# Optimization experiments

Measured on AMD Instinct MI355X. Metric: run time of the kernel, lower is better.

Reference implementation:

```python
import jax, jax.numpy as jnp
import numpy as np

B, S, D, H, F, L, V, SPAN = 4, 1024, 1024, 16, 4096, 4, 32000, 512
DH = D // H
NEG = -1e9


def _ln(x, g, b, eps=1e-12):
    m = x.mean(-1, keepdims=True)
    v = ((x - m) ** 2).mean(-1, keepdims=True)
    return (x - m) * jax.lax.rsqrt(v + eps) * g + b


def setup_inputs() -> dict:
    key = jax.random.key(0)
    ks = iter(jax.random.split(key, 40))
    g = lambda shape: jax.random.normal(next(ks), shape, jnp.float32) * 0.02
    inp = {
        "input_ids": jax.random.randint(next(ks), (B, S), 0, V),
        "segment_ids": jnp.zeros((B, S), jnp.int32),
        "attention_mask": jnp.ones((B, S), jnp.float32),
        "tok_emb": g((V, D)),
        "seg_emb": g((2, D)),
        "emb_ln_g": jnp.ones((D,), jnp.float32),
        "emb_ln_b": jnp.zeros((D,), jnp.float32),
        "rel_emb": g((2 * SPAN, D)),
        "Wq": g((L, D, D)), "bq": jnp.zeros((L, D), jnp.float32),
        "Wk": g((L, D, D)), "bk": jnp.zeros((L, D), jnp.float32),
        "Wv": g((L, D, D)), "bv": jnp.zeros((L, D), jnp.float32),
        "Wo": g((L, D, D)), "bo": jnp.zeros((L, D), jnp.float32),
        "ln1_g": jnp.ones((L, D), jnp.float32), "ln1_b": jnp.zeros((L, D), jnp.float32),
        "W1": g((L, D, F)), "b1": jnp.zeros((L, F), jnp.float32),
        "W2": g((L, F, D)), "b2": jnp.zeros((L, D), jnp.float32),
        "ln2_g": jnp.ones((L, D), jnp.float32), "ln2_b": jnp.zeros((L, D), jnp.float32),
    }
    return inp


def _forward(input_ids, segment_ids, attention_mask, tok_emb, seg_emb, emb_ln_g,
             emb_ln_b, rel_emb, Wq, bq, Wk, bk, Wv, bv, Wo, bo, ln1_g, ln1_b,
             W1, b1, W2, b2, ln2_g, ln2_b):
    # BertEmbedding (max_len=0 => no absolute positions): token + segment, LN, mask
    h = _ln(tok_emb[input_ids] + seg_emb[segment_ids], emb_ln_g, emb_ln_b)
    h = h * attention_mask[..., None]

    # relative positions (bucket_size=0 path): rel[q,k] = q - k, clamped into table
    pos = jnp.arange(S)
    rel = pos[:, None] - pos[None, :]                      # [S,S]
    c2p_idx = jnp.clip(rel + SPAN, 0, 2 * SPAN - 1)        # [S,S]
    p2c_idx = jnp.clip(-rel + SPAN, 0, 2 * SPAN - 1)       # [S,S]
    bias = (1.0 - attention_mask)[:, None, None, :] * NEG  # [B,1,1,S] additive mask

    scale = 1.0 / jnp.sqrt(jnp.asarray(DH * 3, h.dtype))   # scale_factor = 1 + |{c2p,p2c}|

    def layer(h, p):
        wq, bq_, wk, bk_, wv, bv_, wo, bo_, g1, b1n, w1, b1f, w2, b2f, g2, b2n = p
        q = (h @ wq + bq_).reshape(B, S, H, DH)
        k = (h @ wk + bk_).reshape(B, S, H, DH)
        v = (h @ wv + bv_).reshape(B, S, H, DH)
        att = jnp.einsum('bqhd,bkhd->bhqk', q, k) * scale
        # disentangled relative-position bias (shared q/k projections on rel table)
        pos_k = (rel_emb @ wk + bk_).reshape(2 * SPAN, H, DH)
        pos_q = (rel_emb @ wq + bq_).reshape(2 * SPAN, H, DH)
        c2p = jnp.einsum('bqhd,phd->bhqp', q, pos_k) * scale   # [B,H,S,2*SPAN]
        att = att + jnp.take_along_axis(c2p, c2p_idx[None, None], axis=-1)
        p2c = jnp.einsum('bkhd,phd->bhkp', k, pos_q) * scale   # [B,H,S,2*SPAN]
        att = att + jnp.swapaxes(
            jnp.take_along_axis(p2c, p2c_idx[None, None], axis=-1), -1, -2)
        probs = jax.nn.softmax(att + bias, axis=-1)
        ctx = jnp.einsum('bhqk,bkhd->bqhd', probs, v).reshape(B, S, D)
        h = _ln(h + ctx @ wo + bo_, g1, b1n)
        ff = jax.nn.gelu(h @ w1 + b1f, approximate=False) @ w2 + b2f
        return _ln(h + ff, g2, b2n), None

    h, _ = jax.lax.scan(layer, h, (Wq, bq, Wk, bk, Wv, bv, Wo, bo,
                                   ln1_g, ln1_b, W1, b1, W2, b2, ln2_g, ln2_b))
    return h


def reference(input_ids, segment_ids, attention_mask, tok_emb, seg_emb, emb_ln_g,
              emb_ln_b, rel_emb, Wq, bq, Wk, bk, Wv, bv, Wo, bo, ln1_g, ln1_b,
              W1, b1, W2, b2, ln2_g, ln2_b):
    return _forward(input_ids, segment_ids, attention_mask, tok_emb, seg_emb,
                    emb_ln_g, emb_ln_b, rel_emb, Wq, bq, Wk, bk, Wv, bv, Wo, bo,
                    ln1_g, ln1_b, W1, b1, W2, b2, ln2_g, ln2_b)
```

## Files before the change

### kernel.cpp

```cpp
#include <hip/hip_runtime.h>

#define DEV __device__ __forceinline__

typedef __bf16 bf16;
typedef __bf16 bf16x4 __attribute__((ext_vector_type(4)));
typedef __bf16 bf16x8 __attribute__((ext_vector_type(8)));
typedef float f32x4 __attribute__((ext_vector_type(4)));

constexpr int B_ = 4, S_ = 1024, D_ = 1024, H_ = 16, F_ = 4096, L_ = 4, SPAN_ = 512, DH_ = 64;
constexpr float SCALE_ = 0.07216878364870322f;
constexpr float LOG2E_ = 1.4426950408889634f;
constexpr float SCL2_ = SCALE_ * LOG2E_;
constexpr float THR2_ = 11.5f;
constexpr long POSL_ = 32L * 1024 * 64;

DEV void gload_lds16(const void* g, void* l) {
  __builtin_amdgcn_global_load_lds((const __attribute__((address_space(1))) void*)g,
                                   (__attribute__((address_space(3))) void*)l, 16, 0, 0);
}

template <int CTRL>
DEV float dppf(float x) {
  return __builtin_bit_cast(
      float, __builtin_amdgcn_mov_dpp(__builtin_bit_cast(int, x), CTRL, 0xf, 0xf, true));
}
DEV float rowMax16(float v) {
  v = fmaxf(v, dppf<0x128>(v));
  v = fmaxf(v, dppf<0x124>(v));
  v = fmaxf(v, dppf<0x122>(v));
  v = fmaxf(v, dppf<0x121>(v));
  return v;
}
DEV float rowSum16(float v) {
  v += dppf<0x128>(v);
  v += dppf<0x124>(v);
  v += dppf<0x122>(v);
  v += dppf<0x121>(v);
  return v;
}

DEV float blockSum4(float v, volatile float* red) {
#pragma unroll
  for (int o = 32; o; o >>= 1) v += __shfl_xor(v, o);
  if ((threadIdx.x & 63) == 0) red[threadIdx.x >> 6] = v;
  __syncthreads();
  return red[0] + red[1] + red[2] + red[3];
}

DEV bf16x8 lds_frag(const bf16* buf, int row, int chunk) {
  return *(const bf16x8*)((const char*)buf + row * 128 + ((chunk ^ (row & 7)) << 4));
}
DEV bf16x8 rdfrag(const char* base, int row, int chunk) {
  return *(const bf16x8*)(base + row * 128 + ((chunk ^ (row & 7)) << 4));
}

template <int EPI>
__global__ __launch_bounds__(512, 1) void gemm256(
    const bf16* __restrict__ A, const bf16* __restrict__ Bm,
    const float* __restrict__ bias, void* __restrict__ Cout,
    int K, int lda, int ldb, int ldc, long sA, long sB, long sC) {
  extern __shared__ __align__(16) char smem[];

  const int z = blockIdx.z;
  A += (long)z * sA;
  Bm += (long)z * sB;
  const long coff = (long)z * sC;

  const int nwg = gridDim.x * gridDim.y;
  const int flat = blockIdx.y * gridDim.x + blockIdx.x;
  const int qq = nwg >> 3;
  const int swz = (flat & 7) * qq + (flat >> 3);
  const int bx = swz % gridDim.x, by = swz / gridDim.x;
  const int m0 = by * 256, n0 = bx * 256;

  const int tid = threadIdx.x, lane = tid & 63, wave = tid >> 6;
  const int wr = wave >> 2, wc = wave & 3;
  const int fr = lane & 15, fq = lane >> 4;

  f32x4 acc[8][4];
#pragma unroll
  for (int m = 0; m < 8; m++)
#pragma unroll
    for (int n = 0; n < 4; n++) acc[m][n] = f32x4{0.f, 0.f, 0.f, 0.f};

  const int r8 = tid >> 3;
  const int swzel = ((tid & 7) ^ (r8 & 7)) << 3;
  const bf16* ga = A + (long)(m0 + r8) * lda + swzel;
  const bf16* gb = Bm + (long)(n0 + r8) * ldb + swzel;

  const int NT = K >> 6;

  auto stage = [&](int t) {
    const long ko = (long)t * 64;
    char* da = smem + ((t & 1) << 15) + wave * 1024;
    gload_lds16(ga + ko, da);
    gload_lds16(ga + 64 * (long)lda + ko, da + 8192);
    gload_lds16(ga + 128 * (long)lda + ko, da + 16384);
    gload_lds16(ga + 192 * (long)lda + ko, da + 24576);
    char* db = smem + 65536 + ((t & 1) << 15) + wave * 1024;
    gload_lds16(gb + ko, db);
    gload_lds16(gb + 64 * (long)ldb + ko, db + 8192);
    gload_lds16(gb + 128 * (long)ldb + ko, db + 16384);
    gload_lds16(gb + 192 * (long)ldb + ko, db + 24576);
  };

  stage(0);
  asm volatile("s_waitcnt vmcnt(0)" ::: "memory");
  __builtin_amdgcn_s_barrier();

  for (int j = 0; j < NT; j++) {
    const char* Ac = smem + ((j & 1) << 15);
    const char* Bc = smem + 65536 + ((j & 1) << 15);

    if (j + 1 < NT) stage(j + 1);

    bf16x8 af[4][2], bfg[4][2];
#pragma unroll
    for (int m = 0; m < 4; m++) {
      const int ar = wr * 128 + m * 16 + fr;
      af[m][0] = rdfrag(Ac, ar, fq);
      af[m][1] = rdfrag(Ac, ar, 4 + fq);
    }
#pragma unroll
    for (int n = 0; n < 4; n++) {
      const int br = wc * 64 + n * 16 + fr;
      bfg[n][0] = rdfrag(Bc, br, fq);
      bfg[n][1] = rdfrag(Bc, br, 4 + fq);
    }

    __builtin_amdgcn_s_setprio(1);
#pragma unroll
    for (int m = 0; m < 4; m++)
#pragma unroll
      for (int n = 0; n < 4; n++)
#pragma unroll
        for (int kc = 0; kc < 2; kc++)
          acc[m][n] = __builtin_amdgcn_mfma_f32_16x16x32_bf16(af[m][kc], bfg[n][kc],
                                                              acc[m][n], 0, 0, 0);
    __builtin_amdgcn_s_setprio(0);
    __builtin_amdgcn_sched_barrier(0);

#pragma unroll
    for (int m = 0; m < 4; m++) {
      const int ar = wr * 128 + (m + 4) * 16 + fr;
      af[m][0] = rdfrag(Ac, ar, fq);
      af[m][1] = rdfrag(Ac, ar, 4 + fq);
    }
    __builtin_amdgcn_s_setprio(1);
#pragma unroll
    for (int m = 0; m < 4; m++)
#pragma unroll
      for (int n = 0; n < 4; n++)
#pragma unroll
        for (int kc = 0; kc < 2; kc++)
          acc[m + 4][n] = __builtin_amdgcn_mfma_f32_16x16x32_bf16(af[m][kc], bfg[n][kc],
                                                                  acc[m + 4][n], 0, 0, 0);
    __builtin_amdgcn_s_setprio(0);

    asm volatile("s_waitcnt vmcnt(0)" ::: "memory");
    __builtin_amdgcn_s_barrier();
  }

#pragma unroll
  for (int m = 0; m < 8; m++) {
#pragma unroll
    for (int n = 0; n < 4; n++) {
      const int col = n0 + wc * 64 + n * 16 + fr;
      float bval = 0.f;
      if constexpr (EPI == 3 || EPI == 4) bval = bias ? bias[col] : 0.f;
#pragma unroll
      for (int rr = 0; rr < 4; rr++) {
        const int row = m0 + wr * 128 + m * 16 + fq * 4 + rr;
        const long idx = coff + (long)row * ldc + col;
        const float v = acc[m][n][rr];
        if constexpr (EPI == 0) ((float*)Cout)[idx] = v;
        else if constexpr (EPI == 3) ((bf16*)Cout)[idx] = (bf16)(v + bval);
        else if constexpr (EPI == 4) {
          float x = v + bval;
          x = 0.5f * x * (1.f + erff(x * 0.70710678118654752f));
          ((bf16*)Cout)[idx] = (bf16)x;
        }
      }
    }
  }
}

template <int EPI>
__global__ __launch_bounds__(256) void gemm_bt(
    const bf16* __restrict__ A, const bf16* __restrict__ Bm,
    const float* __restrict__ bias, void* __restrict__ Cout,
    int M, int N, int K, int lda, int ldb, int ldc, float alpha,
    long sA, long sB, long sC, long sBias) {
  __shared__ alignas(16) bf16 As[128 * 64];
  __shared__ alignas(16) bf16 Bs[128 * 64];

  const int z = blockIdx.z;
  A += (long)z * sA;
  Bm += (long)z * sB;
  bias += (long)z * sBias;
  const long coff = (long)z * sC;

  const int nwg = gridDim.x * gridDim.y;
  const int flat = blockIdx.y * gridDim.x + blockIdx.x;
  const int qq = nwg >> 3;
  const int swz = (flat & 7) * qq + (flat >> 3);
  const int bx = swz % gridDim.x, by = swz / gridDim.x;

  const int m0 = by * 128, n0 = bx * 128;
  const int tid = threadIdx.x, lane = tid & 63, wave = tid >> 6;
  const int wr = wave >> 1, wc = wave & 1;
  const int fr = lane & 15, fq = lane >> 4;

  f32x4 acc[4][4];
#pragma unroll
  for (int m = 0; m < 4; m++)
#pragma unroll
    for (int n = 0; n < 4; n++) acc[m][n] = f32x4{0.f, 0.f, 0.f, 0.f};

  const int r8 = tid >> 3;
  const int swzel = ((tid & 7) ^ (r8 & 7)) << 3;
  const bf16* ga = A + (long)(m0 + r8) * lda + swzel;
  const bf16* gb = Bm + (long)(n0 + r8) * ldb + swzel;
  const int swzrd = fr & 7;

  for (int k0 = 0; k0 < K; k0 += 64) {
#pragma unroll
    for (int i = 0; i < 4; i++)
      gload_lds16(ga + (long)i * 32 * lda + k0, (char*)As + i * 4096 + wave * 1024);
#pragma unroll
    for (int i = 0; i < 4; i++)
      gload_lds16(gb + (long)i * 32 * ldb + k0, (char*)Bs + i * 4096 + wave * 1024);
    __syncthreads();
#pragma unroll
    for (int kc = 0; kc < 2; kc++) {
      bf16x8 af[4], bfv[4];
#pragma unroll
      for (int m = 0; m < 4; m++)
        af[m] = *(const bf16x8*)((char*)As + (wr * 64 + m * 16 + fr) * 128 +
                                 (((kc * 4 + fq) ^ swzrd) << 4));
#pragma unroll
      for (int n = 0; n < 4; n++)
        bfv[n] = *(const bf16x8*)((char*)Bs + (wc * 64 + n * 16 + fr) * 128 +
                                  (((kc * 4 + fq) ^ swzrd) << 4));
#pragma unroll
      for (int m = 0; m < 4; m++)
#pragma unroll
        for (int n = 0; n < 4; n++)
          acc[m][n] = __builtin_amdgcn_mfma_f32_16x16x32_bf16(af[m], bfv[n], acc[m][n], 0, 0, 0);
    }
    __syncthreads();
  }

#pragma unroll
  for (int m = 0; m < 4; m++) {
#pragma unroll
    for (int n = 0; n < 4; n++) {
      const int col = n0 + wc * 64 + n * 16 + fr;
      float bval = 0.f;
      if constexpr (EPI == 3 || EPI == 4 || EPI == 5) bval = bias ? bias[col] : 0.f;
#pragma unroll
      for (int rr = 0; rr < 4; rr++) {
        const int row = m0 + wr * 64 + m * 16 + fq * 4 + rr;
        const long idx = coff + (long)row * ldc + col;
        const float v = acc[m][n][rr];
        if constexpr (EPI == 0) ((float*)Cout)[idx] = v * alpha;
        else if constexpr (EPI == 3) ((bf16*)Cout)[idx] = (bf16)(v + bval);
        else if constexpr (EPI == 4) {
          float x = v + bval;
          x = 0.5f * x * (1.f + erff(x * 0.70710678118654752f));
          ((bf16*)Cout)[idx] = (bf16)x;
        } else if constexpr (EPI == 5) {
          const long pidx = coff + ((long)(col >> 6) * 1024 + row) * 64 + (col & 63);
          ((bf16*)Cout)[pidx] = (bf16)(v + bval);
        }
      }
    }
  }
}

__global__ __launch_bounds__(256) void repack_kv(const bf16* __restrict__ qkv,
                                                 bf16* __restrict__ kp,
                                                 bf16* __restrict__ vp) {
  const int kt = blockIdx.x, bh = blockIdx.y;
  const int b = bh >> 4, h = bh & 15;
  const int k0 = kt * 64;
  __shared__ bf16 t[64][72];
  const int ty = threadIdx.x >> 3, tx = threadIdx.x & 7;
#pragma unroll
  for (int p = 0; p < 2; p++) {
    const int s = k0 + p * 32 + ty;
    const long base = (long)(b * 1024 + s) * 3072 + h * 64;
    bf16x8 kv = *(const bf16x8*)(qkv + base + 1024 + tx * 8);
    *(bf16x8*)(kp + ((long)(bh * 1024 + s) << 6) + tx * 8) = kv;
    bf16x8 vv = *(const bf16x8*)(qkv + base + 2048 + tx * 8);
    *(bf16x8*)(&t[p * 32 + ty][tx * 8]) = vv;
  }
  __syncthreads();
  const int dh = threadIdx.x >> 2, sc = (threadIdx.x & 3) * 16;
  bf16 tmp[16];
#pragma unroll
  for (int j = 0; j < 16; j++) tmp[j] = t[sc + j][dh];
  bf16* dst = vp + ((long)(bh * 16 + kt) << 12) + dh * 64 + sc;
  *(bf16x8*)dst = *(bf16x8*)tmp;
  *(bf16x8*)(dst + 8) = *(bf16x8*)(tmp + 8);
}

__global__ __launch_bounds__(256) void attn_fused(
    const bf16* __restrict__ qkv, const bf16* __restrict__ kp,
    const bf16* __restrict__ vp, const bf16* __restrict__ pospk,
    const float* __restrict__ mask, bf16* __restrict__ ctx) {
  const int id = blockIdx.x;
  const int xcd = id & 7, sub = id >> 3;
  const int bh = xcd + 8 * (sub >> 4);
  const int qt = sub & 15;
  const int b = bh >> 4, h = bh & 15;
  const int q0 = qt * 64;
  const int tid = threadIdx.x, wave = tid >> 6, lane = tid & 63;
  const int fr = lane & 15, fq = lane >> 4;

  __shared__ alignas(16) char smem[79360];
  bf16* PXk = (bf16*)smem;
  char* p_l = smem;
  bf16* PXq = (bf16*)(smem + 16384);
  bf16* Ks = (bf16*)(smem + 32768);
  bf16* Vs = (bf16*)(smem + 40960);
  bf16* c2p_T = (bf16*)(smem + 49152);
  bf16* p2c_T = (bf16*)(smem + 61952);

  const bf16* posq = pospk + ((long)h << 16);
  const bf16* posk = pospk + ((long)(16 + h) << 16);
  const bf16* kbase = kp + ((long)bh << 16);
  const bf16* vbase = vp + ((long)bh << 16);

  bf16x8 qa[2];
  {
    const bf16* qrow = qkv + (long)(b * 1024 + q0 + wave * 16 + fr) * 3072 + h * 64;
    qa[0] = *(const bf16x8*)(qrow + fq * 8);
    qa[1] = *(const bf16x8*)(qrow + 32 + fq * 8);
  }

  f32x4 o[4];
#pragma unroll
  for (int n = 0; n < 4; n++) o[n] = f32x4{0.f, 0.f, 0.f, 0.f};
  float m_r[4], l_r[4];
#pragma unroll
  for (int r = 0; r < 4; r++) { m_r[r] = -1e30f; l_r[r] = 0.f; }

  char* pl_base = p_l + wave * 2048;
  bf16* c2p_w = c2p_T + wave * 1600;
  const int wbyte = wave * 1024;

  for (int kt = 0; kt < 16; kt++) {
    const int k0 = kt * 64;

    __syncthreads();
    {
      const int j0k = q0 - k0 + 449;
      const int j0q = k0 - q0 + 449;
#pragma unroll
      for (int c = 0; c < 4; c++) {
        const int u = c * 256 + tid;
        const int rr = u >> 3;
        const int sel = (((u & 7) ^ (rr & 7)) << 3);
        int jk = j0k + rr;
        jk = jk < 0 ? 0 : (jk > 1023 ? 1023 : jk);
        gload_lds16(posk + ((long)jk << 6) + sel, (char*)PXk + c * 4096 + wbyte);
        int jq = j0q + rr;
        jq = jq < 0 ? 0 : (jq > 1023 ? 1023 : jq);
        gload_lds16(posq + ((long)jq << 6) + sel, (char*)PXq + c * 4096 + wbyte);
      }
#pragma unroll
      for (int c = 0; c < 2; c++) {
        const int u = c * 256 + tid;
        const int rr = u >> 3;
        const int sel = (((u & 7) ^ (rr & 7)) << 3);
        gload_lds16(kbase + ((long)(k0 + rr) << 6) + sel, (char*)Ks + c * 4096 + wbyte);
        gload_lds16(vbase + ((long)kt << 12) + ((long)rr << 6) + sel,
                    (char*)Vs + c * 4096 + wbyte);
      }
    }
    __syncthreads();

    bf16x8 ka[2];
    ka[0] = lds_frag(Ks, wave * 16 + fr, fq);
    ka[1] = lds_frag(Ks, wave * 16 + fr, 4 + fq);
    __builtin_amdgcn_s_setprio(1);
    {
      f32x4 cw[5];
#pragma unroll
      for (int t = 0; t < 5; t++) cw[t] = f32x4{0.f, 0.f, 0.f, 0.f};
#pragma unroll
      for (int kc = 0; kc < 2; kc++)
#pragma unroll
        for (int t = 0; t < 5; t++) {
          const bf16x8 pb = lds_frag(PXk, wave * 16 + t * 16 + fr, kc * 4 + fq);
          cw[t] = __builtin_amdgcn_mfma_f32_16x16x32_bf16(qa[kc], pb, cw[t], 0, 0, 0);
        }
#pragma unroll
      for (int t = 0; t < 5; t++) {
        bf16x4 pk;
#pragma unroll
        for (int r = 0; r < 4; r++) pk[r] = (bf16)cw[t][r];
        *(bf16x4*)&c2p_w[(t * 16 + fr) * 20 + fq * 4] = pk;
      }
    }
    f32x4 s[4];
#pragma unroll
    for (int n = 0; n < 4; n++) s[n] = f32x4{0.f, 0.f, 0.f, 0.f};
#pragma unroll
    for (int kc = 0; kc < 2; kc++)
#pragma unroll
      for (int n = 0; n < 4; n++) {
        const bf16x8 kb = lds_frag(Ks, n * 16 + fr, kc * 4 + fq);
        s[n] = __builtin_amdgcn_mfma_f32_16x16x32_bf16(qa[kc], kb, s[n], 0, 0, 0);
      }
    {
      f32x4 pw[5];
#pragma unroll
      for (int t = 0; t < 5; t++) pw[t] = f32x4{0.f, 0.f, 0.f, 0.f};
#pragma unroll
      for (int kc = 0; kc < 2; kc++)
#pragma unroll
        for (int t = 0; t < 5; t++) {
          const bf16x8 pb = lds_frag(PXq, (wave + t) * 16 + fr, kc * 4 + fq);
          pw[t] = __builtin_amdgcn_mfma_f32_16x16x32_bf16(ka[kc], pb, pw[t], 0, 0, 0);
        }
#pragma unroll
      for (int t = 0; t < 5; t++) {
        bf16x4 pk;
#pragma unroll
        for (int r = 0; r < 4; r++) pk[r] = (bf16)pw[t][r];
        *(bf16x4*)&p2c_T[((wave + t) * 16 + fr) * 68 + wave * 16 + fq * 4] = pk;
      }
    }
    __builtin_amdgcn_s_setprio(0);
    __syncthreads();

    bf16x8 vb[2][4];
#pragma unroll
    for (int kc = 0; kc < 2; kc++)
#pragma unroll
      for (int n = 0; n < 4; n++) vb[kc][n] = lds_frag(Vs, n * 16 + fr, kc * 4 + fq);

    float st[4][4];
#pragma unroll
    for (int n = 0; n < 4; n++) {
      const int ki = n * 16 + fr;
      const float mb = (1.0f - mask[b * S_ + k0 + ki]) * (-1e9f * LOG2E_);
#pragma unroll
      for (int r = 0; r < 4; r++) {
        const int qi_s = fq * 4 + r;
        const float cv = (float)c2p_w[(qi_s - ki + 63) * 20 + qi_s];
        const float pv = (float)p2c_T[(ki - (wave * 16 + qi_s) + 63) * 68 + ki];
        st[n][r] = (s[n][r] + cv + pv) * SCL2_ + mb;
      }
    }

    float pmax[4];
#pragma unroll
    for (int r = 0; r < 4; r++) {
      float v = fmaxf(fmaxf(st[0][r], st[1][r]), fmaxf(st[2][r], st[3][r]));
      pmax[r] = rowMax16(v);
    }
    const bool ok = (pmax[0] - m_r[0] <= THR2_) && (pmax[1] - m_r[1] <= THR2_) &&
                    (pmax[2] - m_r[2] <= THR2_) && (pmax[3] - m_r[3] <= THR2_);
    if (!__all(ok)) {
#pragma unroll
      for (int r = 0; r < 4; r++) {
        const float mn = fmaxf(m_r[r], pmax[r]);
        const float sc = exp2f(m_r[r] - mn);
        m_r[r] = mn;
        l_r[r] *= sc;
#pragma unroll
        for (int n = 0; n < 4; n++) o[n][r] *= sc;
      }
    }
    float rs[4] = {0.f, 0.f, 0.f, 0.f};
#pragma unroll
    for (int n = 0; n < 4; n++) {
      const int ki = n * 16 + fr;
#pragma unroll
      for (int r = 0; r < 4; r++) {
        const int qi_s = fq * 4 + r;
        const float p = exp2f(st[n][r] - m_r[r]);
        rs[r] += p;
        *(bf16*)(pl_base + qi_s * 128 + ((ki * 2) ^ ((qi_s & 7) << 4))) = (bf16)p;
      }
    }
#pragma unroll
    for (int r = 0; r < 4; r++) l_r[r] += rowSum16(rs[r]);

#pragma unroll
    for (int kc = 0; kc < 2; kc++) {
      const bf16x8 pa =
          *(const bf16x8*)(pl_base + fr * 128 + ((kc * 64 + fq * 16) ^ ((fr & 7) << 4)));
#pragma unroll
      for (int n = 0; n < 4; n++)
        o[n] = __builtin_amdgcn_mfma_f32_16x16x32_bf16(pa, vb[kc][n], o[n], 0, 0, 0);
    }
  }

#pragma unroll
  for (int r = 0; r < 4; r++) {
    const float inv = 1.f / l_r[r];
    const long row = (long)(b * S_ + q0 + wave * 16 + fq * 4 + r) * D_ + h * 64;
#pragma unroll
    for (int n = 0; n < 4; n++) ctx[row + n * 16 + fr] = (bf16)(o[n][r] * inv);
  }
}

__global__ __launch_bounds__(256) void wtrans(const float* __restrict__ W,
                                              bf16* __restrict__ WT, int K, int N,
                                              long sW, long sT) {
  W += (long)blockIdx.z * sW;
  WT += (long)blockIdx.z * sT;
  __shared__ float t[32][33];
  const int n0 = blockIdx.x * 32, k0 = blockIdx.y * 32;
  const int tx = threadIdx.x & 31, ty = threadIdx.x >> 5;
#pragma unroll
  for (int i = ty; i < 32; i += 8) t[i][tx] = W[(long)(k0 + i) * N + n0 + tx];
  __syncthreads();
#pragma unroll
  for (int i = ty; i < 32; i += 8) WT[(long)(n0 + i) * K + k0 + tx] = (bf16)t[tx][i];
}

__global__ __launch_bounds__(256) void f2b(const float* __restrict__ in,
                                           bf16* __restrict__ out, long n) {
  long i = (long)blockIdx.x * 256 + threadIdx.x;
  if (i < n) out[i] = (bf16)in[i];
}

__global__ __launch_bounds__(256) void bias_concat(const float* __restrict__ bq,
                                                   const float* __restrict__ bk,
                                                   const float* __restrict__ bv,
                                                   float* __restrict__ bqkv) {
  const int i = blockIdx.x * 256 + threadIdx.x;
  const int l = i / (3 * D_), s = (i % (3 * D_)) / D_, d = i % D_;
  const float* src = s == 0 ? bq : (s == 1 ? bk : bv);
  bqkv[i] = src[l * D_ + d];
}

__global__ __launch_bounds__(256) void embed_ln(
    const int* __restrict__ ids, const int* __restrict__ segs,
    const float* __restrict__ mask, const float* __restrict__ tok,
    const float* __restrict__ seg, const float* __restrict__ g,
    const float* __restrict__ bta, float* __restrict__ h, bf16* __restrict__ hb) {
  __shared__ float r1[4], r2[4];
  const int t = blockIdx.x;
  const int d4 = threadIdx.x;
  const long tb4 = (long)ids[t] * 256;
  const long sb4 = (long)segs[t] * 256;
  const long b4 = (long)t * 256;
  f32x4 x = ((const f32x4*)tok)[tb4 + d4];
  const f32x4 sv = ((const f32x4*)seg)[sb4 + d4];
#pragma unroll
  for (int r = 0; r < 4; r++) x[r] += sv[r];
  float sm = x[0] + x[1] + x[2] + x[3];
  sm = blockSum4(sm, r1);
  const float mean = sm * (1.f / D_);
  float vs = 0.f;
#pragma unroll
  for (int r = 0; r < 4; r++) {
    const float c = x[r] - mean;
    vs += c * c;
  }
  vs = blockSum4(vs, r2);
  const float rstd = rsqrtf(vs * (1.f / D_) + 1e-12f);
  const float mk = mask[t];
  const f32x4 gv = ((const f32x4*)g)[d4];
  const f32x4 bv = ((const f32x4*)bta)[d4];
  f32x4 y;
  bf16x4 yb;
#pragma unroll
  for (int r = 0; r < 4; r++) {
    y[r] = ((x[r] - mean) * rstd * gv[r] + bv[r]) * mk;
    yb[r] = (bf16)y[r];
  }
  ((f32x4*)h)[b4 + d4] = y;
  *(bf16x4*)&hb[(b4 + d4) * 4] = yb;
}

template <int P>
__global__ __launch_bounds__(256) void ln_residual_red(
    const float* __restrict__ hin, float* __restrict__ hout,
    const float* __restrict__ part, long pstride4,
    const float* __restrict__ bias, const float* __restrict__ g,
    const float* __restrict__ bta, bf16* __restrict__ hb) {
  __shared__ float r1[4], r2[4];
  const int d4 = threadIdx.x;
  const long b4 = (long)blockIdx.x * 256;
  f32x4 x = ((const f32x4*)hin)[b4 + d4];
  const f32x4 bi = ((const f32x4*)bias)[d4];
#pragma unroll
  for (int r = 0; r < 4; r++) x[r] += bi[r];
#pragma unroll
  for (int z = 0; z < P; z++) {
    const f32x4 pv = ((const f32x4*)part)[(long)z * pstride4 + b4 + d4];
#pragma unroll
    for (int r = 0; r < 4; r++) x[r] += pv[r];
  }
  float sm = x[0] + x[1] + x[2] + x[3];
  sm = blockSum4(sm, r1);
  const float mean = sm * (1.f / D_);
  float vs = 0.f;
#pragma unroll
  for (int r = 0; r < 4; r++) {
    const float c = x[r] - mean;
    vs += c * c;
  }
  vs = blockSum4(vs, r2);
  const float rstd = rsqrtf(vs * (1.f / D_) + 1e-12f);
  const f32x4 gv = ((const f32x4*)g)[d4];
  const f32x4 bv = ((const f32x4*)bta)[d4];
  f32x4 y;
  bf16x4 yb;
#pragma unroll
  for (int r = 0; r < 4; r++) {
    y[r] = (x[r] - mean) * rstd * gv[r] + bv[r];
    yb[r] = (bf16)y[r];
  }
  ((f32x4*)hout)[b4 + d4] = y;
  *(bf16x4*)&hb[(b4 + d4) * 4] = yb;
}

extern "C" void kernel_launch(void* const* d_in, const int* in_sizes, int n_in,
                              void* d_out, int out_size, void* d_ws, size_t ws_size,
                              hipStream_t stream) {
  (void)in_sizes; (void)n_in; (void)out_size; (void)ws_size;
  const int* input_ids = (const int*)d_in[0];
  const int* segment_ids = (const int*)d_in[1];
  const float* attention_mask = (const float*)d_in[2];
  const float* tok_emb = (const float*)d_in[3];
  const float* seg_emb = (const float*)d_in[4];
  const float* emb_ln_g = (const float*)d_in[5];
  const float* emb_ln_b = (const float*)d_in[6];
  const float* rel_emb = (const float*)d_in[7];
  const float* Wq = (const float*)d_in[8];
  const float* bq = (const float*)d_in[9];
  const float* Wk = (const float*)d_in[10];
  const float* bk = (const float*)d_in[11];
  const float* Wv = (const float*)d_in[12];
  const float* bv = (const float*)d_in[13];
  const float* Wo = (const float*)d_in[14];
  const float* bo = (const float*)d_in[15];
  const float* ln1_g = (const float*)d_in[16];
  const float* ln1_b = (const float*)d_in[17];
  const float* W1 = (const float*)d_in[18];
  const float* b1 = (const float*)d_in[19];
  const float* W2 = (const float*)d_in[20];
  const float* b2 = (const float*)d_in[21];
  const float* ln2_g = (const float*)d_in[22];
  const float* ln2_b = (const float*)d_in[23];

  const long DD = (long)D_ * D_;
  const long DF = (long)D_ * F_;
  const int D3 = 3 * D_;

  char* ws = (char*)d_ws;
  auto alloc = [&](size_t bytes) {
    char* p = ws;
    ws += (bytes + 255) & ~(size_t)255;
    return p;
  };
  bf16* wqkvT = (bf16*)alloc((size_t)L_ * 3 * DD * 2);
  bf16* woT = (bf16*)alloc((size_t)L_ * DD * 2);
  bf16* w1T = (bf16*)alloc((size_t)L_ * DF * 2);
  bf16* w2T = (bf16*)alloc((size_t)L_ * DF * 2);
  float* bqkv = (float*)alloc((size_t)L_ * 3 * D_ * 4);
  bf16* relb = (bf16*)alloc((size_t)2 * SPAN_ * D_ * 2);
  float* hbuf = (float*)alloc((size_t)B_ * S_ * D_ * 4);
  bf16* hb = (bf16*)alloc((size_t)B_ * S_ * D_ * 2);
  bf16* qkv = (bf16*)alloc((size_t)B_ * S_ * 3 * D_ * 2);
  bf16* kp = (bf16*)alloc((size_t)B_ * H_ * S_ * DH_ * 2);
  bf16* vp = (bf16*)alloc((size_t)B_ * H_ * S_ * DH_ * 2);
  bf16* pospk = (bf16*)alloc((size_t)L_ * POSL_ * 2);
  bf16* ctxb = (bf16*)alloc((size_t)B_ * S_ * D_ * 2);
  bf16* ff1b = (bf16*)alloc((size_t)B_ * S_ * F_ * 2);
  float* kpart = (float*)alloc((size_t)4 * B_ * S_ * D_ * 4);
  const long PSTR = (long)B_ * S_ * D_;

  wtrans<<<dim3(D_ / 32, D_ / 32, L_), 256, 0, stream>>>(Wq, wqkvT + 0 * DD, D_, D_, DD, 3 * DD);
  wtrans<<<dim3(D_ / 32, D_ / 32, L_), 256, 0, stream>>>(Wk, wqkvT + 1 * DD, D_, D_, DD, 3 * DD);
  wtrans<<<dim3(D_ / 32, D_ / 32, L_), 256, 0, stream>>>(Wv, wqkvT + 2 * DD, D_, D_, DD, 3 * DD);
  wtrans<<<dim3(D_ / 32, D_ / 32, L_), 256, 0, stream>>>(Wo, woT, D_, D_, DD, DD);
  wtrans<<<dim3(F_ / 32, D_ / 32, L_), 256, 0, stream>>>(W1, w1T, D_, F_, DF, DF);
  wtrans<<<dim3(D_ / 32, F_ / 32, L_), 256, 0, stream>>>(W2, w2T, F_, D_, DF, DF);
  bias_concat<<<dim3(L_ * 3 * D_ / 256), 256, 0, stream>>>(bq, bk, bv, bqkv);
  f2b<<<dim3((2 * SPAN_ * D_) / 256), 256, 0, stream>>>(rel_emb, relb, (long)2 * SPAN_ * D_);
  gemm_bt<5><<<dim3((2 * D_) / 128, (2 * SPAN_) / 128, L_), 256, 0, stream>>>(
      relb, wqkvT, bqkv, pospk, 2 * SPAN_, 2 * D_, D_, D_, D_, 0, 1.f,
      0, 3 * DD, POSL_, 3 * D_);
  embed_ln<<<dim3(B_ * S_), 256, 0, stream>>>(input_ids, segment_ids, attention_mask,
                                              tok_emb, seg_emb, emb_ln_g, emb_ln_b, hbuf, hb);

  const size_t SH = 131072;

  for (int l = 0; l < L_; ++l) {
    const bf16* wqkv_ = wqkvT + (long)l * 3 * DD;
    const bf16* wo_ = woT + (long)l * DD;
    const bf16* w1_ = w1T + (long)l * DF;
    const bf16* w2_ = w2T + (long)l * DF;
    const float* bqkv_ = bqkv + (long)l * 3 * D_;
    const float* bo_ = bo + (long)l * D_;
    const float* b1_ = b1 + (long)l * F_;
    const float* b2_ = b2 + (long)l * D_;

    gemm_bt<3><<<dim3(D3 / 128, (B_ * S_) / 128, 1), 256, 0, stream>>>(
        hb, wqkv_, bqkv_, qkv, B_ * S_, D3, D_, D_, D_, D3, 1.f, 0, 0, 0, 0);
    repack_kv<<<dim3(16, B_ * H_), 256, 0, stream>>>(qkv, kp, vp);

    attn_fused<<<dim3(1024), 256, 0, stream>>>(qkv, kp, vp, pospk + (long)l * POSL_,
                                               attention_mask, ctxb);

    gemm_bt<0><<<dim3(D_ / 128, (B_ * S_) / 128, 2), 256, 0, stream>>>(
        ctxb, wo_, nullptr, kpart, B_ * S_, D_, D_ / 2, D_, D_, D_, 1.f,
        D_ / 2, D_ / 2, PSTR, 0);
    ln_residual_red<2><<<dim3(B_ * S_), 256, 0, stream>>>(
        hbuf, hbuf, kpart, PSTR / 4, bo_, ln1_g + l * D_, ln1_b + l * D_, hb);

    gemm256<4><<<dim3(F_ / 256, (B_ * S_) / 256, 1), 512, SH, stream>>>(
        hb, w1_, b1_, ff1b, D_, D_, D_, F_, 0, 0, 0);
    gemm256<0><<<dim3(D_ / 256, (B_ * S_) / 256, 4), 512, SH, stream>>>(
        ff1b, w2_, nullptr, kpart, F_ / 4, F_, F_, D_, F_ / 4, F_ / 4, PSTR);
    float* hout = (l == L_ - 1) ? (float*)d_out : hbuf;
    ln_residual_red<4><<<dim3(B_ * S_), 256, 0, stream>>>(
        hbuf, hout, kpart, PSTR / 4, b2_, ln2_g + l * D_, ln2_b + l * D_, hb);
  }
}
```

Before: 1.309 ms.

## Skip relative-position tile work for far-off-diagonal blocks with clamped positions

For key tiles at least ten tiles from the query tile, every relative index clamps to the first or last row of the table. The position terms then reduce to one dot product per query and one per key. These tiles now skip the per-tile position-table loads, the windowed c2p/p2c MFMAs, the LDS transposes and the extra barrier, and compute the two scalar terms with a handful of MFMAs. Separately, K is read straight from the qkv buffer instead of a repacked copy, which shrinks the repack kernel to V only. The cost is more branchy code, strided K loads, and extra register pressure from the fast path.

```diff
diff --git a/kernel.cpp b/kernel.cpp
--- a/kernel.cpp
+++ b/kernel.cpp
@@ -278,9 +278,8 @@
   }
 }
 
-__global__ __launch_bounds__(256) void repack_kv(const bf16* __restrict__ qkv,
-                                                 bf16* __restrict__ kp,
-                                                 bf16* __restrict__ vp) {
+__global__ __launch_bounds__(256) void repack_v(const bf16* __restrict__ qkv,
+                                                bf16* __restrict__ vp) {
   const int kt = blockIdx.x, bh = blockIdx.y;
   const int b = bh >> 4, h = bh & 15;
   const int k0 = kt * 64;
@@ -290,8 +289,6 @@
   for (int p = 0; p < 2; p++) {
     const int s = k0 + p * 32 + ty;
     const long base = (long)(b * 1024 + s) * 3072 + h * 64;
-    bf16x8 kv = *(const bf16x8*)(qkv + base + 1024 + tx * 8);
-    *(bf16x8*)(kp + ((long)(bh * 1024 + s) << 6) + tx * 8) = kv;
     bf16x8 vv = *(const bf16x8*)(qkv + base + 2048 + tx * 8);
     *(bf16x8*)(&t[p * 32 + ty][tx * 8]) = vv;
   }
@@ -306,9 +303,9 @@
 }
 
 __global__ __launch_bounds__(256) void attn_fused(
-    const bf16* __restrict__ qkv, const bf16* __restrict__ kp,
-    const bf16* __restrict__ vp, const bf16* __restrict__ pospk,
-    const float* __restrict__ mask, bf16* __restrict__ ctx) {
+    const bf16* __restrict__ qkv, const bf16* __restrict__ vp,
+    const bf16* __restrict__ pospk, const float* __restrict__ mask,
+    bf16* __restrict__ ctx) {
   const int id = blockIdx.x;
   const int xcd = id & 7, sub = id >> 3;
   const int bh = xcd + 8 * (sub >> 4);
@@ -329,7 +326,7 @@
 
   const bf16* posq = pospk + ((long)h << 16);
   const bf16* posk = pospk + ((long)(16 + h) << 16);
-  const bf16* kbase = kp + ((long)bh << 16);
+  const bf16* kq = qkv + (long)b * 1024 * 3072 + 1024 + h * 64;
   const bf16* vbase = vp + ((long)bh << 16);
 
   bf16x8 qa[2];
@@ -352,9 +349,11 @@
 
   for (int kt = 0; kt < 16; kt++) {
     const int k0 = kt * 64;
+    const int dQK = qt - kt;
+    const bool fast = (dQK >= 10) || (dQK <= -10);
 
     __syncthreads();
-    {
+    if (!fast) {
       const int j0k = q0 - k0 + 449;
       const int j0q = k0 - q0 + 449;
 #pragma unroll
@@ -369,90 +368,130 @@
         jq = jq < 0 ? 0 : (jq > 1023 ? 1023 : jq);
         gload_lds16(posq + ((long)jq << 6) + sel, (char*)PXq + c * 4096 + wbyte);
       }
-#pragma unroll
-      for (int c = 0; c < 2; c++) {
-        const int u = c * 256 + tid;
-        const int rr = u >> 3;
-        const int sel = (((u & 7) ^ (rr & 7)) << 3);
-        gload_lds16(kbase + ((long)(k0 + rr) << 6) + sel, (char*)Ks + c * 4096 + wbyte);
-        gload_lds16(vbase + ((long)kt << 12) + ((long)rr << 6) + sel,
-                    (char*)Vs + c * 4096 + wbyte);
-      }
+    }
+#pragma unroll
+    for (int c = 0; c < 2; c++) {
+      const int u = c * 256 + tid;
+      const int rr = u >> 3;
+      const int sel = (((u & 7) ^ (rr & 7)) << 3);
+      gload_lds16(kq + (long)(k0 + rr) * 3072 + sel, (char*)Ks + c * 4096 + wbyte);
+      gload_lds16(vbase + ((long)kt << 12) + ((long)rr << 6) + sel,
+                  (char*)Vs + c * 4096 + wbyte);
     }
     __syncthreads();
 
-    bf16x8 ka[2];
-    ka[0] = lds_frag(Ks, wave * 16 + fr, fq);
-    ka[1] = lds_frag(Ks, wave * 16 + fr, 4 + fq);
-    __builtin_amdgcn_s_setprio(1);
-    {
-      f32x4 cw[5];
-#pragma unroll
-      for (int t = 0; t < 5; t++) cw[t] = f32x4{0.f, 0.f, 0.f, 0.f};
+    f32x4 s[4];
+#pragma unroll
+    for (int n = 0; n < 4; n++) s[n] = f32x4{0.f, 0.f, 0.f, 0.f};
+    f32x4 qd = f32x4{0.f, 0.f, 0.f, 0.f};
+    f32x4 kda[4];
+#pragma unroll
+    for (int n = 0; n < 4; n++) kda[n] = f32x4{0.f, 0.f, 0.f, 0.f};
+
+    if (fast) {
+      const bf16* pkB = (dQK >= 10) ? posk + (1023 << 6) : posk;
+      const bf16* pqB = (dQK >= 10) ? posq : posq + (1023 << 6);
+      bf16x8 pkf[2], pqf[2];
+#pragma unroll
+      for (int kc = 0; kc < 2; kc++) {
+        pkf[kc] = *(const bf16x8*)(pkB + kc * 32 + fq * 8);
+        pqf[kc] = *(const bf16x8*)(pqB + kc * 32 + fq * 8);
+      }
+      __builtin_amdgcn_s_setprio(1);
+#pragma unroll
+      for (int kc = 0; kc < 2; kc++) {
+        qd = __builtin_amdgcn_mfma_f32_16x16x32_bf16(qa[kc], pkf[kc], qd, 0, 0, 0);
+#pragma unroll
+        for (int n = 0; n < 4; n++) {
+          const bf16x8 kb = lds_frag(Ks, n * 16 + fr, kc * 4 + fq);
+          s[n] = __builtin_amdgcn_mfma_f32_16x16x32_bf16(qa[kc], kb, s[n], 0, 0, 0);
+          kda[n] = __builtin_amdgcn_mfma_f32_16x16x32_bf16(pqf[kc], kb, kda[n], 0, 0, 0);
+        }
+      }
+      __builtin_amdgcn_s_setprio(0);
+    } else {
+      bf16x8 ka[2];
+      ka[0] = lds_frag(Ks, wave * 16 + fr, fq);
+      ka[1] = lds_frag(Ks, wave * 16 + fr, 4 + fq);
+      __builtin_amdgcn_s_setprio(1);
+      {
+        f32x4 cw[5];
+#pragma unroll
+        for (int t = 0; t < 5; t++) cw[t] = f32x4{0.f, 0.f, 0.f, 0.f};
+#pragma unroll
+        for (int kc = 0; kc < 2; kc++)
+#pragma unroll
+          for (int t = 0; t < 5; t++) {
+            const bf16x8 pb = lds_frag(PXk, wave * 16 + t * 16 + fr, kc * 4 + fq);
+            cw[t] = __builtin_amdgcn_mfma_f32_16x16x32_bf16(qa[kc], pb, cw[t], 0, 0, 0);
+          }
+#pragma unroll
+        for (int t = 0; t < 5; t++) {
+          bf16x4 pk;
+#pragma unroll
+          for (int r = 0; r < 4; r++) pk[r] = (bf16)cw[t][r];
+          *(bf16x4*)&c2p_w[(t * 16 + fr) * 20 + fq * 4] = pk;
+        }
+      }
 #pragma unroll
       for (int kc = 0; kc < 2; kc++)
 #pragma unroll
+        for (int n = 0; n < 4; n++) {
+          const bf16x8 kb = lds_frag(Ks, n * 16 + fr, kc * 4 + fq);
+          s[n] = __builtin_amdgcn_mfma_f32_16x16x32_bf16(qa[kc], kb, s[n], 0, 0, 0);
+        }
+      {
+        f32x4 pw[5];
+#pragma unroll
+        for (int t = 0; t < 5; t++) pw[t] = f32x4{0.f, 0.f, 0.f, 0.f};
+#pragma unroll
+        for (int kc = 0; kc < 2; kc++)
+#pragma unroll
+          for (int t = 0; t < 5; t++) {
+            const bf16x8 pb = lds_frag(PXq, (wave + t) * 16 + fr, kc * 4 + fq);
+            pw[t] = __builtin_amdgcn_mfma_f32_16x16x32_bf16(ka[kc], pb, pw[t], 0, 0, 0);
+          }
+#pragma unroll
         for (int t = 0; t < 5; t++) {
-          const bf16x8 pb = lds_frag(PXk, wave * 16 + t * 16 + fr, kc * 4 + fq);
-          cw[t] = __builtin_amdgcn_mfma_f32_16x16x32_bf16(qa[kc], pb, cw[t], 0, 0, 0);
+          bf16x4 pk;
+#pragma unroll
+          for (int r = 0; r < 4; r++) pk[r] = (bf16)pw[t][r];
+          *(bf16x4*)&p2c_T[((wave + t) * 16 + fr) * 68 + wave * 16 + fq * 4] = pk;
         }
-#pragma unroll
-      for (int t = 0; t < 5; t++) {
-        bf16x4 pk;
-#pragma unroll
-        for (int r = 0; r < 4; r++) pk[r] = (bf16)cw[t][r];
-        *(bf16x4*)&c2p_w[(t * 16 + fr) * 20 + fq * 4] = pk;
-      }
-    }
-    f32x4 s[4];
-#pragma unroll
-    for (int n = 0; n < 4; n++) s[n] = f32x4{0.f, 0.f, 0.f, 0.f};
+      }
+      __builtin_amdgcn_s_setprio(0);
+      __syncthreads();
+    }
+
+    bf16x8 vb[2][4];
 #pragma unroll
     for (int kc = 0; kc < 2; kc++)
 #pragma unroll
+      for (int n = 0; n < 4; n++) vb[kc][n] = lds_frag(Vs, n * 16 + fr, kc * 4 + fq);
+
+    float st[4][4];
+    if (fast) {
+#pragma unroll
       for (int n = 0; n < 4; n++) {
-        const bf16x8 kb = lds_frag(Ks, n * 16 + fr, kc * 4 + fq);
-        s[n] = __builtin_amdgcn_mfma_f32_16x16x32_bf16(qa[kc], kb, s[n], 0, 0, 0);
-      }
-    {
-      f32x4 pw[5];
-#pragma unroll
-      for (int t = 0; t < 5; t++) pw[t] = f32x4{0.f, 0.f, 0.f, 0.f};
-#pragma unroll
-      for (int kc = 0; kc < 2; kc++)
-#pragma unroll
-        for (int t = 0; t < 5; t++) {
-          const bf16x8 pb = lds_frag(PXq, (wave + t) * 16 + fr, kc * 4 + fq);
-          pw[t] = __builtin_amdgcn_mfma_f32_16x16x32_bf16(ka[kc], pb, pw[t], 0, 0, 0);
+        const int ki = n * 16 + fr;
+        const float mb = (1.0f - mask[b * S_ + k0 + ki]) * (-1e9f * LOG2E_);
+        const float kd = kda[n][0];
+#pragma unroll
+        for (int r = 0; r < 4; r++)
+          st[n][r] = (s[n][r] + qd[r] + kd) * SCL2_ + mb;
+      }
+    } else {
+#pragma unroll
+      for (int n = 0; n < 4; n++) {
+        const int ki = n * 16 + fr;
+        const float mb = (1.0f - mask[b * S_ + k0 + ki]) * (-1e9f * LOG2E_);
+#pragma unroll
+        for (int r = 0; r < 4; r++) {
+          const int qi_s = fq * 4 + r;
+          const float cv = (float)c2p_w[(qi_s - ki + 63) * 20 + qi_s];
+          const float pv = (float)p2c_T[(ki - (wave * 16 + qi_s) + 63) * 68 + ki];
+          st[n][r] = (s[n][r] + cv + pv) * SCL2_ + mb;
         }
-#pragma unroll
-      for (int t = 0; t < 5; t++) {
-        bf16x4 pk;
-#pragma unroll
-        for (int r = 0; r < 4; r++) pk[r] = (bf16)pw[t][r];
-        *(bf16x4*)&p2c_T[((wave + t) * 16 + fr) * 68 + wave * 16 + fq * 4] = pk;
-      }
-    }
-    __builtin_amdgcn_s_setprio(0);
-    __syncthreads();
-
-    bf16x8 vb[2][4];
-#pragma unroll
-    for (int kc = 0; kc < 2; kc++)
-#pragma unroll
-      for (int n = 0; n < 4; n++) vb[kc][n] = lds_frag(Vs, n * 16 + fr, kc * 4 + fq);
-
-    float st[4][4];
-#pragma unroll
-    for (int n = 0; n < 4; n++) {
-      const int ki = n * 16 + fr;
-      const float mb = (1.0f - mask[b * S_ + k0 + ki]) * (-1e9f * LOG2E_);
-#pragma unroll
-      for (int r = 0; r < 4; r++) {
-        const int qi_s = fq * 4 + r;
-        const float cv = (float)c2p_w[(qi_s - ki + 63) * 20 + qi_s];
-        const float pv = (float)p2c_T[(ki - (wave * 16 + qi_s) + 63) * 68 + ki];
-        st[n][r] = (s[n][r] + cv + pv) * SCL2_ + mb;
       }
     }
 
@@ -671,7 +710,6 @@
   float* hbuf = (float*)alloc((size_t)B_ * S_ * D_ * 4);
   bf16* hb = (bf16*)alloc((size_t)B_ * S_ * D_ * 2);
   bf16* qkv = (bf16*)alloc((size_t)B_ * S_ * 3 * D_ * 2);
-  bf16* kp = (bf16*)alloc((size_t)B_ * H_ * S_ * DH_ * 2);
   bf16* vp = (bf16*)alloc((size_t)B_ * H_ * S_ * DH_ * 2);
   bf16* pospk = (bf16*)alloc((size_t)L_ * POSL_ * 2);
   bf16* ctxb = (bf16*)alloc((size_t)B_ * S_ * D_ * 2);
@@ -707,9 +745,9 @@
 
     gemm_bt<3><<<dim3(D3 / 128, (B_ * S_) / 128, 1), 256, 0, stream>>>(
         hb, wqkv_, bqkv_, qkv, B_ * S_, D3, D_, D_, D_, D3, 1.f, 0, 0, 0, 0);
-    repack_kv<<<dim3(16, B_ * H_), 256, 0, stream>>>(qkv, kp, vp);
-
-    attn_fused<<<dim3(1024), 256, 0, stream>>>(qkv, kp, vp, pospk + (long)l * POSL_,
+    repack_v<<<dim3(16, B_ * H_), 256, 0, stream>>>(qkv, vp);
+
+    attn_fused<<<dim3(1024), 256, 0, stream>>>(qkv, vp, pospk + (long)l * POSL_,
                                                attention_mask, ctxb);
 
     gemm_bt<0><<<dim3(D_ / 128, (B_ * S_) / 128, 2), 256, 0, stream>>>(
```

Measured after the change: 1.500 ms. +14.5%, slower.
